# Kernel optimization log

Hardware: AMD Instinct MI355X
Metric: run time of the kernel (lower is better)

## Reference

```python
import jax, jax.numpy as jnp
import numpy as np

DIM = 1024
HEADS = 16
DIM_HEAD = DIM // HEADS
SCALE = DIM_HEAD ** -0.5
LN_EPS = 1e-5


def setup_inputs() -> dict:
    key = jax.random.key(0)
    ks = jax.random.split(key, 10)
    b, n, m = 2, 2048, 2048
    s = 0.02
    return {
        "x": jax.random.normal(ks[0], (b, n, DIM), jnp.float32),
        "context": jax.random.normal(ks[1], (b, m, DIM), jnp.float32),
        "alibi": jax.random.normal(ks[2], (HEADS, n, m), jnp.float32),
        "Wq": jax.random.normal(ks[3], (DIM, DIM), jnp.float32) * s,
        "Wk": jax.random.normal(ks[4], (DIM, DIM), jnp.float32) * s,
        "Wv": jax.random.normal(ks[5], (DIM, DIM), jnp.float32) * s,
        "Wo": jax.random.normal(ks[6], (DIM, DIM), jnp.float32) * s,
        "bo": jnp.zeros((DIM,), jnp.float32),
        "ln_w": jnp.ones((DIM,), jnp.float32),
        "ln_b": jnp.zeros((DIM,), jnp.float32),
    }


def _layernorm(t, w, b):
    mu = jnp.mean(t, axis=-1, keepdims=True)
    var = jnp.var(t, axis=-1, keepdims=True)
    return (t - mu) * jax.lax.rsqrt(var + LN_EPS) * w + b


def reference(x, context, alibi, Wq, Wk, Wv, Wo, bo, ln_w, ln_b):
    xn = _layernorm(x, ln_w, ln_b)
    cn = _layernorm(context, ln_w, ln_b)
    # torch Linear: y = x @ W.T
    q = xn @ Wq.T
    k = cn @ Wk.T
    v = cn @ Wv.T
    b, n, _ = q.shape
    m = k.shape[1]
    # b n (h d) -> b h n d
    q = q.reshape(b, n, HEADS, DIM_HEAD).transpose(0, 2, 1, 3)
    k = k.reshape(b, m, HEADS, DIM_HEAD).transpose(0, 2, 1, 3)
    v = v.reshape(b, m, HEADS, DIM_HEAD).transpose(0, 2, 1, 3)
    scores = jnp.einsum("bhid,bhjd->bhij", q, k) * SCALE + alibi
    attn = jax.nn.softmax(scores, axis=-1)
    out = jnp.einsum("bhij,bhjd->bhid", attn, v)
    out = out.transpose(0, 2, 1, 3).reshape(b, n, HEADS * DIM_HEAD)
    return out @ Wo.T + bo
```

## Files before the change

kernel.cpp:

```cpp
#include <hip/hip_runtime.h>
#include <stdint.h>

#define DIM 1024
#define HEADS 16
#define DHEAD 64
#define LN_EPS 1e-5f
#define SCALE 0.125f
#define LOG2E 1.44269504089f
#define SMAX 4.0f

typedef _Float16 h8 __attribute__((ext_vector_type(8)));
typedef _Float16 h4 __attribute__((ext_vector_type(4)));
typedef _Float16 h2 __attribute__((ext_vector_type(2)));
typedef float f32x4 __attribute__((ext_vector_type(4)));

typedef __attribute__((address_space(1))) void* as1p;
typedef __attribute__((address_space(3))) void* as3p;

__device__ __forceinline__ void gl_lds16(const void* g, void* l) {
  __builtin_amdgcn_global_load_lds((as1p)g, (as3p)l, 16, 0, 0);
}

__device__ __forceinline__ float wave_sum(float v) {
#pragma unroll
  for (int o = 32; o > 0; o >>= 1) v += __shfl_xor(v, o, 64);
  return v;
}

__global__ __launch_bounds__(256) void cast4_kernel(const float* __restrict__ W0,
                                                    const float* __restrict__ W1,
                                                    const float* __restrict__ W2,
                                                    const float* __restrict__ W3,
                                                    _Float16* __restrict__ dst) {
  int gi = blockIdx.x * 256 + threadIdx.x;
  int wsel = gi >> 18;
  int li = gi & 0x3FFFF;
  const float* s = W0;
  if (wsel == 1) s = W1;
  else if (wsel == 2) s = W2;
  else if (wsel == 3) s = W3;
  float4 f = ((const float4*)s)[li];
  h4 o;
  o[0] = (_Float16)f.x; o[1] = (_Float16)f.y;
  o[2] = (_Float16)f.z; o[3] = (_Float16)f.w;
  ((h4*)dst)[gi] = o;
}

__global__ __launch_bounds__(256) void ln_f16(const float* __restrict__ x,
                                              const float* __restrict__ context,
                                              _Float16* __restrict__ out,
                                              const float* __restrict__ w,
                                              const float* __restrict__ b) {
  int row = blockIdx.x;
  const float* src = (row < 4096) ? x : context;
  int srow = row & 4095;
  const float4* rp = (const float4*)(src + (size_t)srow * DIM);
  float4 v = rp[threadIdx.x];
  float s = v.x + v.y + v.z + v.w;
  float ss = fmaf(v.x, v.x, fmaf(v.y, v.y, fmaf(v.z, v.z, v.w * v.w)));
  s = wave_sum(s);
  ss = wave_sum(ss);
  __shared__ float red[8];
  int wid = threadIdx.x >> 6, lane = threadIdx.x & 63;
  if (lane == 0) { red[wid] = s; red[4 + wid] = ss; }
  __syncthreads();
  s = red[0] + red[1] + red[2] + red[3];
  ss = red[4] + red[5] + red[6] + red[7];
  float mu = s * (1.0f / DIM);
  float var = ss * (1.0f / DIM) - mu * mu;
  float inv = rsqrtf(var + LN_EPS);
  float4 wv = ((const float4*)w)[threadIdx.x];
  float4 bv = ((const float4*)b)[threadIdx.x];
  h4 o;
  o[0] = (_Float16)((v.x - mu) * inv * wv.x + bv.x);
  o[1] = (_Float16)((v.y - mu) * inv * wv.y + bv.y);
  o[2] = (_Float16)((v.z - mu) * inv * wv.z + bv.z);
  o[3] = (_Float16)((v.w - mu) * inv * wv.w + bv.w);
  *(h4*)(out + (size_t)row * DIM + 4 * threadIdx.x) = o;
}

template <int OUT_MODE>
__device__ __forceinline__ void gemm_core128(const _Float16* __restrict__ A,
                                             const _Float16* __restrict__ W,
                                             void* __restrict__ C,
                                             const float* __restrict__ bias,
                                             int rowBase, int colBase) {
  __shared__ _Float16 As[128 * 64];
  __shared__ _Float16 Bs[128 * 64];
  int tid = threadIdx.x;
  int w = tid >> 6, lane = tid & 63;
  int quad = lane >> 4, l15 = lane & 15;
  int wr = w >> 1, wc = w & 1;
  f32x4 acc[4][4] = {};

  for (int k0 = 0; k0 < DIM; k0 += 64) {
#pragma unroll
    for (int l = 0; l < 4; l++) {
      int id = l * 256 + tid;
      int row = id & 127, c = id >> 7;
      gl_lds16(A + (size_t)(rowBase + row) * DIM + k0 + c * 8,
               &As[(l * 256 + w * 64) * 8]);
    }
#pragma unroll
    for (int l = 0; l < 4; l++) {
      int id = l * 256 + tid;
      int row = id & 127, c = id >> 7;
      gl_lds16(W + (size_t)(colBase + row) * DIM + k0 + c * 8,
               &Bs[(l * 256 + w * 64) * 8]);
    }
    __syncthreads();

    h8 af[2][4], bf[2][4];
#pragma unroll
    for (int ks = 0; ks < 2; ks++) {
#pragma unroll
      for (int mg = 0; mg < 4; mg++)
        af[ks][mg] = *(const h8*)&As[((ks * 4 + quad) * 128 + wr * 64 + mg * 16 + l15) * 8];
#pragma unroll
      for (int ng = 0; ng < 4; ng++)
        bf[ks][ng] = *(const h8*)&Bs[((ks * 4 + quad) * 128 + wc * 64 + ng * 16 + l15) * 8];
    }
#pragma unroll
    for (int mg = 0; mg < 4; mg++)
#pragma unroll
      for (int ng = 0; ng < 4; ng++)
#pragma unroll
        for (int ks = 0; ks < 2; ks++)
          acc[mg][ng] = __builtin_amdgcn_mfma_f32_16x16x32_f16(af[ks][mg], bf[ks][ng], acc[mg][ng], 0, 0, 0);
    __syncthreads();
  }

#pragma unroll
  for (int mg = 0; mg < 4; mg++)
#pragma unroll
    for (int ng = 0; ng < 4; ng++) {
      int ccol = colBase + wc * 64 + ng * 16 + l15;
      float bv = (OUT_MODE == 1) ? bias[ccol] : 0.f;
#pragma unroll
      for (int r = 0; r < 4; r++) {
        int crow = rowBase + wr * 64 + mg * 16 + quad * 4 + r;
        if (OUT_MODE == 0)
          ((_Float16*)C)[(size_t)crow * DIM + ccol] = (_Float16)acc[mg][ng][r];
        else
          ((float*)C)[(size_t)crow * DIM + ccol] = acc[mg][ng][r] + bv;
      }
    }
}

__global__ __launch_bounds__(256) void gemm_qkv(const _Float16* __restrict__ xnh,
                                                const _Float16* __restrict__ cnh,
                                                const _Float16* __restrict__ wq,
                                                const _Float16* __restrict__ wk,
                                                const _Float16* __restrict__ wv,
                                                _Float16* __restrict__ q,
                                                _Float16* __restrict__ k,
                                                _Float16* __restrict__ v) {
  int z = blockIdx.z;
  const _Float16* A = (z == 0) ? xnh : cnh;
  const _Float16* W = (z == 0) ? wq : (z == 1) ? wk : wv;
  _Float16* C = (z == 0) ? q : (z == 1) ? k : v;
  gemm_core128<0>(A, W, C, nullptr, blockIdx.y * 128, blockIdx.x * 128);
}

__global__ __launch_bounds__(256) void gemm_out(const _Float16* __restrict__ A,
                                                const _Float16* __restrict__ W,
                                                float* __restrict__ C,
                                                const float* __restrict__ bias) {
  gemm_core128<1>(A, W, C, bias, blockIdx.y * 128, blockIdx.x * 128);
}

__global__ __launch_bounds__(512) void attn_mfma(const _Float16* __restrict__ q,
                                                 const _Float16* __restrict__ k,
                                                 const _Float16* __restrict__ v,
                                                 const float* __restrict__ alibi,
                                                 _Float16* __restrict__ out) {
  __shared__ _Float16 Ks[2][2][64 * 64];
  __shared__ _Float16 Vt[2][2][64][72];
  __shared__ _Float16 Ps[2][8][16][72];

  int tid = threadIdx.x;
  int w = tid >> 6, lane = tid & 63;
  int quad = lane >> 4, l15 = lane & 15;
  int qbase = blockIdx.x * 128;
  int h = blockIdx.y;

  const _Float16 qs = (_Float16)(SCALE * LOG2E);
  h8 qf[2][2];
#pragma unroll
  for (int bi = 0; bi < 2; bi++) {
    const _Float16* qp = q + (size_t)(bi * 2048 + qbase + w * 16 + l15) * DIM + h * DHEAD;
    qf[bi][0] = *(const h8*)(qp + quad * 8) * qs;
    qf[bi][1] = *(const h8*)(qp + 32 + quad * 8) * qs;
  }

  h8 ones;
#pragma unroll
  for (int i = 0; i < 8; i++) ones[i] = (_Float16)1.0f;

  const float NEG_M2 = -SMAX * LOG2E;
  f32x4 l_acc[2] = {};
  f32x4 o_acc[2][4] = {};

  const float* arow_base = alibi + (size_t)h * 2048 * 2048 +
                           (size_t)(qbase + w * 16 + quad * 4) * 2048;

  int vbi = tid >> 8, vtt = tid & 255, vm = vtt & 15, vdg = vtt >> 4;

  float av[4][4];
#pragma unroll
  for (int r = 0; r < 4; r++)
#pragma unroll
    for (int ng = 0; ng < 4; ng++)
      av[r][ng] = arow_base[(size_t)r * 2048 + ng * 16 + l15];

#pragma unroll
  for (int l = 0; l < 2; l++) {
    int idx = w * 2 + l, sbi = idx >> 3, c = idx & 7;
    gl_lds16(k + (size_t)(sbi * 2048 + lane) * DIM + h * DHEAD + c * 8,
             &Ks[sbi][0][(c * 64) * 8]);
  }
  {
    const _Float16* vs = v + (size_t)(vbi * 2048 + vm) * DIM + h * DHEAD + vdg * 4;
    h4 a0 = *(const h4*)(vs);
    h4 a1 = *(const h4*)(vs + 16 * DIM);
    h4 a2 = *(const h4*)(vs + 32 * DIM);
    h4 a3 = *(const h4*)(vs + 48 * DIM);
#pragma unroll
    for (int i = 0; i < 4; i++) {
      h4 pk; pk[0] = a0[i]; pk[1] = a1[i]; pk[2] = a2[i]; pk[3] = a3[i];
      *(h4*)&Vt[vbi][0][vdg * 4 + i][4 * vm] = pk;
    }
  }
  __syncthreads();

  for (int t = 0; t < 32; t++) {
    int buf = t & 1;
    float avn[4][4];
    if (t + 1 < 32) {
      int kb1 = (t + 1) * 64;
#pragma unroll
      for (int l = 0; l < 2; l++) {
        int idx = w * 2 + l, sbi = idx >> 3, c = idx & 7;
        gl_lds16(k + (size_t)(sbi * 2048 + kb1 + lane) * DIM + h * DHEAD + c * 8,
                 &Ks[sbi][buf ^ 1][(c * 64) * 8]);
      }
      const _Float16* vs = v + (size_t)(vbi * 2048 + kb1 + vm) * DIM + h * DHEAD + vdg * 4;
      h4 a0 = *(const h4*)(vs);
      h4 a1 = *(const h4*)(vs + 16 * DIM);
      h4 a2 = *(const h4*)(vs + 32 * DIM);
      h4 a3 = *(const h4*)(vs + 48 * DIM);
#pragma unroll
      for (int i = 0; i < 4; i++) {
        h4 pk; pk[0] = a0[i]; pk[1] = a1[i]; pk[2] = a2[i]; pk[3] = a3[i];
        *(h4*)&Vt[vbi][buf ^ 1][vdg * 4 + i][4 * vm] = pk;
      }
#pragma unroll
      for (int r = 0; r < 4; r++)
#pragma unroll
        for (int ng = 0; ng < 4; ng++)
          avn[r][ng] = arow_base[(size_t)r * 2048 + kb1 + ng * 16 + l15];
    }

#pragma unroll
    for (int bi = 0; bi < 2; bi++) {
      f32x4 s_acc[4];
#pragma unroll
      for (int ng = 0; ng < 4; ng++) {
        s_acc[ng][0] = NEG_M2; s_acc[ng][1] = NEG_M2;
        s_acc[ng][2] = NEG_M2; s_acc[ng][3] = NEG_M2;
      }
#pragma unroll
      for (int ng = 0; ng < 4; ng++)
#pragma unroll
        for (int ks = 0; ks < 2; ks++) {
          h8 bfr = *(const h8*)&Ks[bi][buf][((ks * 4 + quad) * 64 + ng * 16 + l15) * 8];
          s_acc[ng] = __builtin_amdgcn_mfma_f32_16x16x32_f16(qf[bi][ks], bfr, s_acc[ng], 0, 0, 0);
        }

#pragma unroll
      for (int r = 0; r < 4; r++) {
        h4 pk;
#pragma unroll
        for (int ng = 0; ng < 4; ng++)
          pk[ng] = (_Float16)exp2f(fmaf(av[r][ng], LOG2E, s_acc[ng][r]));
        *(h4*)&Ps[bi][w][quad * 4 + r][4 * l15] = pk;
      }

      h8 pf[2];
      pf[0] = *(const h8*)&Ps[bi][w][l15][quad * 8];
      pf[1] = *(const h8*)&Ps[bi][w][l15][32 + quad * 8];
      l_acc[bi] = __builtin_amdgcn_mfma_f32_16x16x32_f16(pf[0], ones, l_acc[bi], 0, 0, 0);
      l_acc[bi] = __builtin_amdgcn_mfma_f32_16x16x32_f16(pf[1], ones, l_acc[bi], 0, 0, 0);
#pragma unroll
      for (int ngd = 0; ngd < 4; ngd++)
#pragma unroll
        for (int ks = 0; ks < 2; ks++) {
          h8 vf = *(const h8*)&Vt[bi][buf][ngd * 16 + l15][ks * 32 + quad * 8];
          o_acc[bi][ngd] = __builtin_amdgcn_mfma_f32_16x16x32_f16(pf[ks], vf, o_acc[bi][ngd], 0, 0, 0);
        }
    }

#pragma unroll
    for (int r = 0; r < 4; r++)
#pragma unroll
      for (int ng = 0; ng < 4; ng++) av[r][ng] = avn[r][ng];

    __syncthreads();
  }

#pragma unroll
  for (int bi = 0; bi < 2; bi++)
#pragma unroll
    for (int ngd = 0; ngd < 4; ngd++)
#pragma unroll
      for (int r = 0; r < 4; r++) {
        int iq = qbase + w * 16 + quad * 4 + r;
        out[(size_t)(bi * 2048 + iq) * DIM + h * DHEAD + ngd * 16 + l15] =
            (_Float16)(o_acc[bi][ngd][r] / l_acc[bi][r]);
      }
}

extern "C" void kernel_launch(void* const* d_in, const int* in_sizes, int n_in,
                              void* d_out, int out_size, void* d_ws, size_t ws_size,
                              hipStream_t stream) {
  const float* x = (const float*)d_in[0];
  const float* context = (const float*)d_in[1];
  const float* alibi = (const float*)d_in[2];
  const float* Wq = (const float*)d_in[3];
  const float* Wk = (const float*)d_in[4];
  const float* Wv = (const float*)d_in[5];
  const float* Wo = (const float*)d_in[6];
  const float* bo = (const float*)d_in[7];
  const float* ln_w = (const float*)d_in[8];
  const float* ln_b = (const float*)d_in[9];
  float* out = (float*)d_out;

  const size_t WSZ = (size_t)DIM * DIM;
  const size_t MSZ = (size_t)4096 * DIM;
  _Float16* ws16 = (_Float16*)d_ws;
  _Float16* wq_h = ws16;
  _Float16* wk_h = wq_h + WSZ;
  _Float16* wv_h = wk_h + WSZ;
  _Float16* wo_h = wv_h + WSZ;
  _Float16* xnh = wo_h + WSZ;
  _Float16* cnh = xnh + MSZ;
  _Float16* qh = cnh + MSZ;
  _Float16* kh = qh + MSZ;
  _Float16* vh = kh + MSZ;
  _Float16* aoh = vh + MSZ;

  cast4_kernel<<<4096, 256, 0, stream>>>(Wq, Wk, Wv, Wo, wq_h);
  ln_f16<<<8192, 256, 0, stream>>>(x, context, xnh, ln_w, ln_b);

  dim3 gqkv(8, 32, 3);
  gemm_qkv<<<gqkv, 256, 0, stream>>>(xnh, cnh, wq_h, wk_h, wv_h, qh, kh, vh);

  dim3 ag(16, HEADS);
  attn_mfma<<<ag, 512, 0, stream>>>(qh, kh, vh, alibi, aoh);

  dim3 go(8, 32);
  gemm_out<<<go, 256, 0, stream>>>(aoh, wo_h, out, bo);
}
```

Before: 549.6 us.

## Replace QKV GEMM with 256x256-tile kernel using a ping-pong LDS pipeline

Replaces the 128x128-tile QKV projection GEMM with a 512-thread kernel that computes 256x256 output tiles. It stages tiles with direct global-to-LDS loads into double-buffered slots and interleaves the LDS fragment reads, the next-tile staging and the MFMA groups with fine-grained barriers and priority hints. The aim is more data reuse per loaded byte and better overlap of memory traffic with matrix math. In exchange the grid shrinks to 192 blocks, fewer than the number of CUs, and each block holds a large LDS footprint, so occupancy and load balance may suffer.

Result: faster. 528.3 us (-3.9%).

```diff
diff --git a/kernel.cpp b/kernel.cpp
--- a/kernel.cpp
+++ b/kernel.cpp
@@ -147,26 +147,150 @@
     }
 }
 
-__global__ __launch_bounds__(256) void gemm_qkv(const _Float16* __restrict__ xnh,
-                                                const _Float16* __restrict__ cnh,
-                                                const _Float16* __restrict__ wq,
-                                                const _Float16* __restrict__ wk,
-                                                const _Float16* __restrict__ wv,
-                                                _Float16* __restrict__ q,
-                                                _Float16* __restrict__ k,
-                                                _Float16* __restrict__ v) {
-  int z = blockIdx.z;
-  const _Float16* A = (z == 0) ? xnh : cnh;
-  const _Float16* W = (z == 0) ? wq : (z == 1) ? wk : wv;
-  _Float16* C = (z == 0) ? q : (z == 1) ? k : v;
-  gemm_core128<0>(A, W, C, nullptr, blockIdx.y * 128, blockIdx.x * 128);
-}
-
 __global__ __launch_bounds__(256) void gemm_out(const _Float16* __restrict__ A,
                                                 const _Float16* __restrict__ W,
                                                 float* __restrict__ C,
                                                 const float* __restrict__ bias) {
   gemm_core128<1>(A, W, C, bias, blockIdx.y * 128, blockIdx.x * 128);
+}
+
+
+#define G256_BAR __builtin_amdgcn_s_barrier()
+#define G256_WV4 asm volatile("s_waitcnt vmcnt(4)" ::: "memory")
+#define G256_WL0 asm volatile("s_waitcnt lgkmcnt(0)" ::: "memory")
+
+#define G256_STG(matIsB, b, h, t)                                              \
+  do {                                                                         \
+    const _Float16* _src = (matIsB) ? Wbase : Abase;                           \
+    int _slot = (matIsB) * 4 + (b) * 2 + (h);                                  \
+    int _k0 = ((t) & 15) * 64;                                                 \
+    gl_lds16(_src + (size_t)(h) * 128 * DIM + _k0 + sc * 8,                    \
+             &lds[_slot * 8192 + (sc * 128 + rh64) * 8]);                      \
+    gl_lds16(_src + (size_t)(h) * 128 * DIM + _k0 + (sc + 4) * 8,              \
+             &lds[_slot * 8192 + ((sc + 4) * 128 + rh64) * 8]);                \
+  } while (0)
+
+#define G256_LDA(dst, b, mh)                                                   \
+  do {                                                                         \
+    _Pragma("unroll") for (int ks = 0; ks < 2; ks++)                           \
+        _Pragma("unroll") for (int m = 0; m < 4; m++)                          \
+            dst[ks][m] = *(const h8*)&lds[((b) * 2 + wr) * 8192 +              \
+                ((ks * 4 + quad) * 128 + (mh) * 64 + m * 16 + l15) * 8];       \
+  } while (0)
+
+#define G256_LDB(dst, b, nh)                                                   \
+  do {                                                                         \
+    _Pragma("unroll") for (int ks = 0; ks < 2; ks++)                           \
+        _Pragma("unroll") for (int n = 0; n < 2; n++)                          \
+            dst[ks][n] = *(const h8*)&lds[(4 + (b) * 2 + (wc >> 1)) * 8192 +   \
+                ((ks * 4 + quad) * 128 + (wc & 1) * 64 +                       \
+                 ((nh) * 2 + n) * 16 + l15) * 8];                              \
+  } while (0)
+
+#define G256_MM(a_, b_, mh, nh)                                                \
+  do {                                                                         \
+    __builtin_amdgcn_s_setprio(1);                                             \
+    _Pragma("unroll") for (int m = 0; m < 4; m++)                              \
+        _Pragma("unroll") for (int n = 0; n < 2; n++)                          \
+            _Pragma("unroll") for (int ks = 0; ks < 2; ks++)                   \
+                acc[(mh) * 4 + m][(nh) * 2 + n] =                              \
+                    __builtin_amdgcn_mfma_f32_16x16x32_f16(                    \
+                        a_[ks][m], b_[ks][n], acc[(mh) * 4 + m][(nh) * 2 + n], \
+                        0, 0, 0);                                              \
+    __builtin_amdgcn_s_setprio(0);                                             \
+  } while (0)
+
+__global__ __launch_bounds__(512, 2) void gemm_qkv256(
+    const _Float16* __restrict__ xnh, const _Float16* __restrict__ cnh,
+    const _Float16* __restrict__ wq, const _Float16* __restrict__ wk,
+    const _Float16* __restrict__ wv, _Float16* __restrict__ qo,
+    _Float16* __restrict__ ko, _Float16* __restrict__ vo) {
+  int z = blockIdx.z;
+  const _Float16* A = (z == 0) ? xnh : cnh;
+  const _Float16* W = (z == 0) ? wq : (z == 1) ? wk : wv;
+  _Float16* C = (z == 0) ? qo : (z == 1) ? ko : vo;
+  int rowBase = blockIdx.y * 256, colBase = blockIdx.x * 256;
+
+  __shared__ __align__(16) _Float16 lds[8 * 8192];
+  int tid = threadIdx.x;
+  int w = tid >> 6, lane = tid & 63;
+  int quad = lane >> 4, l15 = lane & 15;
+  int wr = w >> 2, wc = w & 3;
+
+  int sc = w >> 1;
+  int rh64 = (w & 1) * 64;
+  const _Float16* Abase = A + (size_t)(rowBase + rh64 + lane) * DIM;
+  const _Float16* Wbase = W + (size_t)(colBase + rh64 + lane) * DIM;
+
+  f32x4 acc[8][4] = {};
+  h8 af[2][4], bf0[2][2], bf1[2][2];
+
+  G256_STG(1, 0, 0, 0);
+  G256_STG(1, 0, 1, 0);
+  G256_STG(0, 0, 0, 0);
+  G256_STG(0, 0, 1, 0);
+  G256_STG(1, 1, 0, 1);
+  G256_STG(1, 1, 1, 1);
+  G256_WV4;
+  G256_BAR;
+
+  for (int i = 0; i < 8; i++) {
+    int t1 = 2 * i + 1, t2 = 2 * i + 2, t3 = 2 * i + 3;
+    G256_LDA(af, 0, 0);
+    G256_LDB(bf0, 0, 0);
+    G256_STG(0, 1, 0, t1);
+    G256_BAR; G256_WL0;
+    G256_MM(af, bf0, 0, 0);
+    G256_BAR;
+    G256_LDB(bf1, 0, 1);
+    G256_STG(0, 1, 1, t1);
+    G256_BAR; G256_WL0;
+    G256_MM(af, bf1, 0, 1);
+    G256_BAR;
+    G256_LDA(af, 0, 1);
+    G256_STG(1, 0, 0, t2);
+    G256_BAR; G256_WL0;
+    G256_MM(af, bf1, 1, 1);
+    G256_BAR;
+    G256_STG(1, 0, 1, t2);
+    G256_BAR;
+    G256_MM(af, bf0, 1, 0);
+    G256_WV4;
+    G256_BAR;
+    G256_LDA(af, 1, 0);
+    G256_LDB(bf0, 1, 0);
+    G256_STG(0, 0, 0, t2);
+    G256_BAR; G256_WL0;
+    G256_MM(af, bf0, 0, 0);
+    G256_BAR;
+    G256_LDB(bf1, 1, 1);
+    G256_STG(0, 0, 1, t2);
+    G256_BAR; G256_WL0;
+    G256_MM(af, bf1, 0, 1);
+    G256_BAR;
+    G256_LDA(af, 1, 1);
+    G256_STG(1, 1, 0, t3);
+    G256_BAR; G256_WL0;
+    G256_MM(af, bf1, 1, 1);
+    G256_BAR;
+    G256_STG(1, 1, 1, t3);
+    G256_BAR;
+    G256_MM(af, bf0, 1, 0);
+    G256_WV4;
+    G256_BAR;
+  }
+
+#pragma unroll
+  for (int m8 = 0; m8 < 8; m8++)
+#pragma unroll
+    for (int n4 = 0; n4 < 4; n4++) {
+      int ccol = colBase + wc * 64 + n4 * 16 + l15;
+#pragma unroll
+      for (int r = 0; r < 4; r++) {
+        int crow = rowBase + wr * 128 + m8 * 16 + quad * 4 + r;
+        C[(size_t)crow * DIM + ccol] = (_Float16)acc[m8][n4][r];
+      }
+    }
 }
 
 __global__ __launch_bounds__(512) void attn_mfma(const _Float16* __restrict__ q,
@@ -352,8 +476,8 @@
   cast4_kernel<<<4096, 256, 0, stream>>>(Wq, Wk, Wv, Wo, wq_h);
   ln_f16<<<8192, 256, 0, stream>>>(x, context, xnh, ln_w, ln_b);
 
-  dim3 gqkv(8, 32, 3);
-  gemm_qkv<<<gqkv, 256, 0, stream>>>(xnh, cnh, wq_h, wk_h, wv_h, qh, kh, vh);
+  dim3 gqkv(4, 16, 3);
+  gemm_qkv256<<<gqkv, 512, 0, stream>>>(xnh, cnh, wq_h, wk_h, wv_h, qh, kh, vh);
 
   dim3 ag(16, HEADS);
   attn_mfma<<<ag, 512, 0, stream>>>(qh, kh, vh, alibi, aoh);
```
